# Kernel tuning notes

Measured on AMD Instinct MI355X. Metric: run time of the kernel, lower is better.

## Reference

```python
import jax, jax.numpy as jnp
import numpy as np

B, N, D, H, DEPTH = 2, 2048, 768, 12, 4
DH = D // H
SCALE = DH ** -0.5
EPS = 1e-5
FF = 4 * D


def layer_norm(x, w, b):
    m = jnp.mean(x, axis=-1, keepdims=True)
    v = jnp.mean((x - m) ** 2, axis=-1, keepdims=True)
    return (x - m) * jax.lax.rsqrt(v + EPS) * w + b


def to_heads(t):  # [b, n, D] -> [b, H, n, DH]
    b, n, _ = t.shape
    return t.reshape(b, n, H, DH).transpose(0, 2, 1, 3)


def merge_heads(t):  # [b, H, n, DH] -> [b, n, D]
    b, h, n, dh = t.shape
    return t.transpose(0, 2, 1, 3).reshape(b, n, D)


def attend(q, k, v, bias):
    s = jnp.einsum('bhid,bhjd->bhij', q, k) * SCALE + bias
    a = jax.nn.softmax(s, axis=-1)
    return merge_heads(jnp.einsum('bhij,bhjd->bhid', a, v))


def setup_inputs():
    key = jax.random.key(0)
    ks = iter(jax.random.split(key, 16))

    def p(shape, scale=0.02):
        return jax.random.normal(next(ks), shape, dtype=jnp.float32) * scale

    inp = {
        'x': jax.random.normal(next(ks), (B, N, D), dtype=jnp.float32),
        'context': jax.random.normal(next(ks), (B, N, D), dtype=jnp.float32),
        'relative_position_bias': jax.random.normal(next(ks), (1, H, N, N), dtype=jnp.float32) * 0.02,
        # self-attn params (stacked over depth)
        'ln1_w': jnp.ones((DEPTH, D), jnp.float32), 'ln1_b': jnp.zeros((DEPTH, D), jnp.float32),
        'w_qkv': p((DEPTH, D, 3 * D)),
        'w_so': p((DEPTH, D, D)), 'b_so': jnp.zeros((DEPTH, D), jnp.float32),
        # cross-attn params (shared LN applied to x and context, as in source)
        'ln2_w': jnp.ones((DEPTH, D), jnp.float32), 'ln2_b': jnp.zeros((DEPTH, D), jnp.float32),
        'w_q': p((DEPTH, D, D)), 'w_k': p((DEPTH, D, D)), 'w_v': p((DEPTH, D, D)),
        'w_co': p((DEPTH, D, D)), 'b_co': jnp.zeros((DEPTH, D), jnp.float32),
        # FFN params
        'ln3_w': jnp.ones((DEPTH, D), jnp.float32), 'ln3_b': jnp.zeros((DEPTH, D), jnp.float32),
        'w_f1': p((DEPTH, D, FF)), 'b_f1': jnp.zeros((DEPTH, FF), jnp.float32),
        'w_f2': p((DEPTH, FF, D)), 'b_f2': jnp.zeros((DEPTH, D), jnp.float32),
        # final norm
        'lnout_w': jnp.ones((D,), jnp.float32), 'lnout_b': jnp.zeros((D,), jnp.float32),
    }
    return inp


def reference(x, context, relative_position_bias,
              ln1_w, ln1_b, w_qkv, w_so, b_so,
              ln2_w, ln2_b, w_q, w_k, w_v, w_co, b_co,
              ln3_w, ln3_b, w_f1, b_f1, w_f2, b_f2,
              lnout_w, lnout_b):
    bias = relative_position_bias
    for i in range(DEPTH):
        # self-attention block (pre-norm, residual)
        xn = layer_norm(x, ln1_w[i], ln1_b[i])
        q, k, v = jnp.split(xn @ w_qkv[i], 3, axis=-1)
        o = attend(to_heads(q), to_heads(k), to_heads(v), bias)
        x = o @ w_so[i] + b_so[i] + x
        # cross-attention block (input_norm shared for x and context)
        xn = layer_norm(x, ln2_w[i], ln2_b[i])
        cn = layer_norm(context, ln2_w[i], ln2_b[i])
        o = attend(to_heads(xn @ w_q[i]), to_heads(cn @ w_k[i]), to_heads(cn @ w_v[i]), bias)
        x = o @ w_co[i] + b_co[i] + x
        # FFN block
        xn = layer_norm(x, ln3_w[i], ln3_b[i])
        h = jax.nn.gelu(xn @ w_f1[i] + b_f1[i], approximate=False)
        x = h @ w_f2[i] + b_f2[i] + x
    return layer_norm(x, lnout_w, lnout_b)
```

## Files before the change

### kernel.cpp

```cpp
#include <hip/hip_runtime.h>
#include <cstdint>
#include <cstddef>

#define DEV static __device__ __forceinline__

typedef float  f32x4 __attribute__((ext_vector_type(4)));
typedef short  s16x8 __attribute__((ext_vector_type(8)));
typedef unsigned short u16;
typedef unsigned short u16x2 __attribute__((ext_vector_type(2)));
typedef unsigned short u16x4 __attribute__((ext_vector_type(4)));
typedef __bf16 bf16x8 __attribute__((ext_vector_type(8)));

#define LOG2E 1.4426950408889634f
#define QSCALE_CONST 0.18033688011112042f

DEV float bf2f(u16 v){ union { unsigned u; float f; } x; x.u = ((unsigned)v) << 16; return x.f; }
DEV u16 f2bf(float f){ return __builtin_bit_cast(u16, (__bf16)f); }

DEV float fexp2(float x){
#if __has_builtin(__builtin_amdgcn_exp2f)
  return __builtin_amdgcn_exp2f(x);
#else
  return exp2f(x);
#endif
}

DEV f32x4 mfma16(s16x8 a, s16x8 b, f32x4 c){
  return __builtin_amdgcn_mfma_f32_16x16x32_bf16(
      __builtin_bit_cast(bf16x8, a), __builtin_bit_cast(bf16x8, b), c, 0, 0, 0);
}

DEV void gld16(const void* g, void* l){
  __builtin_amdgcn_global_load_lds(
      (const __attribute__((address_space(1))) void*)(uintptr_t)g,
      (__attribute__((address_space(3))) void*)(unsigned)(uintptr_t)l,
      16, 0, 0);
}

__global__ void __launch_bounds__(256)
transpose_cvt(const float* __restrict__ src, u16* __restrict__ dst, int K, int N,
              size_t dzstride){
  int z = blockIdx.z;
  src += (size_t)z * K * N;
  dst += (size_t)z * dzstride;
  __shared__ float t[32][33];
  int n0 = blockIdx.x * 32, k0 = blockIdx.y * 32;
#pragma unroll
  for (int i = 0; i < 4; ++i)
    t[threadIdx.y + 8*i][threadIdx.x] = src[(size_t)(k0 + threadIdx.y + 8*i) * N + n0 + threadIdx.x];
  __syncthreads();
#pragma unroll
  for (int i = 0; i < 4; ++i)
    dst[(size_t)(n0 + threadIdx.y + 8*i) * K + k0 + threadIdx.x] = f2bf(t[threadIdx.x][threadIdx.y + 8*i]);
}

__global__ void __launch_bounds__(256)
cvt_bias(const float* __restrict__ in, u16* __restrict__ out){
  size_t i = ((size_t)blockIdx.x * 256 + threadIdx.x) * 4;
  f32x4 v = *(const f32x4*)(in + i);
  u16x4 o;
#pragma unroll
  for (int j = 0; j < 4; ++j) o[j] = f2bf(v[j] * LOG2E);
  *(u16x4*)(out + i) = o;
}

template<typename OUT>
__global__ void __launch_bounds__(256)
ln_kernel(const float* __restrict__ x0, const float* __restrict__ x1,
          const float* __restrict__ w, const float* __restrict__ bsh,
          OUT* __restrict__ o0, OUT* __restrict__ o1){
  int row = blockIdx.x, tid = threadIdx.x;
  const float* xr; OUT* orow;
  if (row < 4096){ xr = x0 + (size_t)row * 768; orow = o0 + (size_t)row * 768; }
  else           { xr = x1 + (size_t)(row - 4096) * 768; orow = o1 + (size_t)(row - 4096) * 768; }
  float v0 = xr[tid], v1 = xr[tid + 256], v2 = xr[tid + 512];
  float s = v0 + v1 + v2, s2 = v0*v0 + v1*v1 + v2*v2;
#pragma unroll
  for (int off = 1; off < 64; off <<= 1){ s += __shfl_xor(s, off); s2 += __shfl_xor(s2, off); }
  __shared__ float red[8];
  int wid = tid >> 6;
  if ((tid & 63) == 0){ red[wid] = s; red[wid + 4] = s2; }
  __syncthreads();
  s  = red[0] + red[1] + red[2] + red[3];
  s2 = red[4] + red[5] + red[6] + red[7];
  float m = s * (1.f/768.f);
  float var = s2 * (1.f/768.f) - m * m;
  float rstd = rsqrtf(var + 1e-5f);
#pragma unroll
  for (int i = 0; i < 3; ++i){
    int c = tid + 256 * i;
    float vv = (i == 0 ? v0 : (i == 1 ? v1 : v2));
    float o = (vv - m) * rstd * w[c] + bsh[c];
    if constexpr (sizeof(OUT) == 2) orow[c] = f2bf(o);
    else                            orow[c] = o;
  }
}

template<int BN, int EPI>
__global__ void __launch_bounds__(256)
gemm_bf16(const u16* __restrict__ A, int lda, const u16* __restrict__ Bt, int ldb,
          int nk, u16* __restrict__ Cb, float* __restrict__ Cf, int ldc,
          const float* __restrict__ bias, const float* __restrict__ resid,
          const u16* __restrict__ A2, const u16* __restrict__ Bt2){
  constexpr int NT = BN / 32;
  __shared__ u16 As[2][128 * 32];
  __shared__ u16 Bs[2][BN * 32];
  float colscale = 1.0f;
  if constexpr (EPI == 4){
    const int z = blockIdx.z;
    if (z == 0){ colscale = QSCALE_CONST; }
    else { A = A2; Bt = Bt2 + (size_t)(z - 1) * 768 * 768; }
    Cb += z * 768;
  }
  const int tid = threadIdx.x, w = tid >> 6, lane = tid & 63;
  const int l16 = lane & 15, g = lane >> 4;
  const int m0 = blockIdx.x * 128, n0 = blockIdx.y * BN;
  const int wm = (w >> 1) * 64, wn = (w & 1) * (BN / 2);
  f32x4 acc[4][NT] = {};

  const int L0 = w * 1024 + lane * 16;
  const int L1 = (w + 4) * 1024 + lane * 16;
  const u16* a0 = A + (size_t)(m0 + (L0 >> 6)) * lda + ((L0 & 63) >> 1);
  const u16* a1 = A + (size_t)(m0 + (L1 >> 6)) * lda + ((L1 & 63) >> 1);
  const u16* b0; const u16* b1 = nullptr;
  if constexpr (BN == 128){
    b0 = Bt + (size_t)(n0 + (L0 >> 6)) * ldb + ((L0 & 63) >> 1);
    b1 = Bt + (size_t)(n0 + (L1 >> 6)) * ldb + ((L1 & 63) >> 1);
  } else {
    const int Lb = tid * 16;
    b0 = Bt + (size_t)(n0 + (Lb >> 6)) * ldb + ((Lb & 63) >> 1);
  }

  {
    char* ab = (char*)As[0]; char* bb = (char*)Bs[0];
    gld16(a0, ab + w * 1024); gld16(a1, ab + (w + 4) * 1024);
    if constexpr (BN == 128){ gld16(b0, bb + w * 1024); gld16(b1, bb + (w + 4) * 1024); }
    else                    { gld16(b0, bb + w * 1024); }
  }
  __syncthreads();

  int cb = 0;
  for (int kt = 0; kt < nk; ++kt){
    if (kt + 1 < nk){
      const int k1 = (kt + 1) * 32;
      char* ab = (char*)As[cb ^ 1]; char* bb = (char*)Bs[cb ^ 1];
      gld16(a0 + k1, ab + w * 1024); gld16(a1 + k1, ab + (w + 4) * 1024);
      if constexpr (BN == 128){ gld16(b0 + k1, bb + w * 1024); gld16(b1 + k1, bb + (w + 4) * 1024); }
      else                    { gld16(b0 + k1, bb + w * 1024); }
    }

    const u16* Ab = As[cb]; const u16* Bb = Bs[cb];
    s16x8 af[4], bfv[NT];
#pragma unroll
    for (int mi = 0; mi < 4; ++mi)
      af[mi] = *(const s16x8*)(Ab + (wm + mi*16 + l16) * 32 + 8 * g);
#pragma unroll
    for (int ni = 0; ni < NT; ++ni)
      bfv[ni] = *(const s16x8*)(Bb + (wn + ni*16 + l16) * 32 + 8 * g);
#pragma unroll
    for (int mi = 0; mi < 4; ++mi)
#pragma unroll
      for (int ni = 0; ni < NT; ++ni)
        acc[mi][ni] = mfma16(af[mi], bfv[ni], acc[mi][ni]);

    __syncthreads();
    cb ^= 1;
  }

#pragma unroll
  for (int mi = 0; mi < 4; ++mi){
    const int rg = m0 + wm + mi*16 + 4*g;
#pragma unroll
    for (int ni = 0; ni < NT; ++ni){
      const int col = n0 + wn + ni*16 + l16;
      f32x4 v = acc[mi][ni];
#pragma unroll
      for (int r = 0; r < 4; ++r){
        const int row = rg + r;
        if constexpr (EPI == 0){
          Cb[(size_t)row * ldc + col] = f2bf(v[r]);
        } else if constexpr (EPI == 1){
          Cf[(size_t)row * ldc + col] = v[r] + bias[col] + resid[(size_t)row * ldc + col];
        } else if constexpr (EPI == 2){
          float t = v[r] + bias[col];
          float ge = 0.5f * t * (1.0f + erff(t * 0.7071067811865476f));
          Cb[(size_t)row * ldc + col] = f2bf(ge);
        } else if constexpr (EPI == 3){
          float sc = (col < 768) ? QSCALE_CONST : 1.0f;
          Cb[(size_t)row * ldc + col] = f2bf(v[r] * sc);
        } else {
          Cb[(size_t)row * ldc + col] = f2bf(v[r] * colscale);
        }
      }
    }
  }
}

__global__ void __launch_bounds__(256)
attn_kernel(const u16* __restrict__ qkv, const u16* __restrict__ bias, u16* __restrict__ out){
  __shared__ __align__(16) u16 Ks[2][4096];
  __shared__ __align__(16) u16 Vt[2][4096];
  __shared__ __align__(16) u16 Pl[4][1024];

  const int tid = threadIdx.x, w = tid >> 6, lane = tid & 63;
  const int l16 = lane & 15, g = lane >> 4;
  const int qt = blockIdx.x, h = blockIdx.y, b = blockIdx.z;
  const int rowbase = b * 2048, q0 = qt * 64;

  const int ci0 = w * 64 + lane, ci1 = ci0 + 256;
  const int r0 = ci0 >> 3, sc0 = ci0 & 7, r1 = ci1 >> 3, sc1 = ci1 & 7;
  const u16* kp0 = qkv + (size_t)(rowbase + r0) * 2304 + 768 + h * 64 + (((sc0 ^ (r0 & 7)) & 7) << 3);
  const u16* kp1 = qkv + (size_t)(rowbase + r1) * 2304 + 768 + h * 64 + (((sc1 ^ (r1 & 7)) & 7) << 3);
  const int dh0 = (tid & 31) * 2, vs = tid >> 5;
  const u16* vp = qkv + (size_t)(rowbase + vs * 8) * 2304 + 1536 + h * 64 + dh0;
  u16x2 vr[8];
  const u16* bptr = bias + ((size_t)h * 2048 + q0 + w * 16 + l16) * 2048 + 4 * g;
  u16x4 brc[4], brn[4];

  const u16* qrow = qkv + (size_t)(rowbase + q0 + w * 16 + l16) * 2304 + h * 64;
  s16x8 qf0 = *(const s16x8*)(qrow + 8 * g);
  s16x8 qf1 = *(const s16x8*)(qrow + 32 + 8 * g);

  f32x4 oacc[4] = {};
  float mrun = -3.0e38f, lrun = 0.f;
  const int sw = l16 & 7;

  {
    char* kb = (char*)Ks[0] + w * 1024;
    gld16(kp0, kb); gld16(kp1, kb + 4096);
#pragma unroll
    for (int i = 0; i < 8; ++i) vr[i] = *(const u16x2*)(vp + (size_t)i * 2304);
#pragma unroll
    for (int mi = 0; mi < 4; ++mi) brc[mi] = *(const u16x4*)(bptr + 16 * mi);
    s16x8 vA, vB;
#pragma unroll
    for (int j = 0; j < 8; ++j){ vA[j] = (short)vr[j][0]; vB[j] = (short)vr[j][1]; }
    *(s16x8*)(Vt[0] + dh0 * 64 + ((vs ^ (dh0 & 7)) << 3)) = vA;
    *(s16x8*)(Vt[0] + (dh0 + 1) * 64 + ((vs ^ ((dh0 + 1) & 7)) << 3)) = vB;
  }
  __syncthreads();

  for (int t = 0; t < 32; ++t){
    const int cb = t & 1;
    if (t < 31){
      const size_t koff = (size_t)(t + 1) * 64 * 2304;
      char* kb = (char*)Ks[cb ^ 1] + w * 1024;
      gld16(kp0 + koff, kb); gld16(kp1 + koff, kb + 4096);
      const u16* p = vp + koff;
#pragma unroll
      for (int i = 0; i < 8; ++i) vr[i] = *(const u16x2*)(p + (size_t)i * 2304);
      const u16* bp = bptr + (t + 1) * 64;
#pragma unroll
      for (int mi = 0; mi < 4; ++mi) brn[mi] = *(const u16x4*)(bp + 16 * mi);
    }

    f32x4 st[4];
#pragma unroll
    for (int mi = 0; mi < 4; ++mi){
      const int row = l16 + 16 * mi;
      s16x8 kf0 = *(const s16x8*)(Ks[cb] + row * 64 + ((g ^ sw) << 3));
      s16x8 kf1 = *(const s16x8*)(Ks[cb] + row * 64 + (((g + 4) ^ sw) << 3));
      f32x4 z = {};
      z = mfma16(kf0, qf0, z);
      st[mi] = mfma16(kf1, qf1, z);
    }

    float tmax = -3.0e38f;
#pragma unroll
    for (int mi = 0; mi < 4; ++mi){
#pragma unroll
      for (int r = 0; r < 4; ++r){
        float v = st[mi][r] + bf2f(brc[mi][r]);
        st[mi][r] = v;
        tmax = fmaxf(tmax, v);
      }
    }
    tmax = fmaxf(tmax, __shfl_xor(tmax, 16));
    tmax = fmaxf(tmax, __shfl_xor(tmax, 32));
    if (!__all(tmax <= mrun + 8.f)){
      float mnew = fmaxf(mrun, tmax);
      float al = fexp2(mrun - mnew);
      mrun = mnew;
      lrun *= al;
#pragma unroll
      for (int r = 0; r < 4; ++r){
        float aq = __shfl(al, 4 * g + r);
#pragma unroll
        for (int ni = 0; ni < 4; ++ni) oacc[ni][r] *= aq;
      }
    }
    float ssum = 0.f;
#pragma unroll
    for (int mi = 0; mi < 4; ++mi){
      u16x4 pk;
#pragma unroll
      for (int r = 0; r < 4; ++r){
        float pv = fexp2(st[mi][r] - mrun);
        ssum += pv;
        pk[r] = f2bf(pv);
      }
      *(u16x4*)(Pl[w] + l16 * 64 + (((2*mi + (g >> 1)) ^ sw) << 3) + 4 * (g & 1)) = pk;
    }
    ssum += __shfl_xor(ssum, 16);
    ssum += __shfl_xor(ssum, 32);
    lrun += ssum;

#pragma unroll
    for (int ks2 = 0; ks2 < 2; ++ks2){
      s16x8 pf = *(const s16x8*)(Pl[w] + l16 * 64 + (((4*ks2 + g) ^ sw) << 3));
#pragma unroll
      for (int ni = 0; ni < 4; ++ni){
        const int dh = l16 + 16 * ni;
        s16x8 vf = *(const s16x8*)(Vt[cb] + dh * 64 + (((4*ks2 + g) ^ sw) << 3));
        oacc[ni] = mfma16(pf, vf, oacc[ni]);
      }
    }

    if (t < 31){
      s16x8 vA, vB;
#pragma unroll
      for (int j = 0; j < 8; ++j){ vA[j] = (short)vr[j][0]; vB[j] = (short)vr[j][1]; }
      *(s16x8*)(Vt[cb ^ 1] + dh0 * 64 + ((vs ^ (dh0 & 7)) << 3)) = vA;
      *(s16x8*)(Vt[cb ^ 1] + (dh0 + 1) * 64 + ((vs ^ ((dh0 + 1) & 7)) << 3)) = vB;
#pragma unroll
      for (int mi = 0; mi < 4; ++mi) brc[mi] = brn[mi];
    }
    __syncthreads();
  }

#pragma unroll
  for (int r = 0; r < 4; ++r){
    float lq = __shfl(lrun, 4 * g + r);
    float inv = 1.0f / lq;
    const int row = rowbase + q0 + w * 16 + 4 * g + r;
#pragma unroll
    for (int ni = 0; ni < 4; ++ni)
      out[(size_t)row * 768 + h * 64 + l16 + 16 * ni] = f2bf(oacc[ni][r] * inv);
  }
}

extern "C" void kernel_launch(void* const* d_in, const int* in_sizes, int n_in,
                              void* d_out, int out_size, void* d_ws, size_t ws_size,
                              hipStream_t stream){
  const float* in_x    = (const float*)d_in[0];
  const float* in_ctx  = (const float*)d_in[1];
  const float* in_bias = (const float*)d_in[2];
  const float* ln1_w = (const float*)d_in[3];
  const float* ln1_b = (const float*)d_in[4];
  const float* w_qkv = (const float*)d_in[5];
  const float* w_so  = (const float*)d_in[6];
  const float* b_so  = (const float*)d_in[7];
  const float* ln2_w = (const float*)d_in[8];
  const float* ln2_b = (const float*)d_in[9];
  const float* w_q   = (const float*)d_in[10];
  const float* w_k   = (const float*)d_in[11];
  const float* w_v   = (const float*)d_in[12];
  const float* w_co  = (const float*)d_in[13];
  const float* b_co  = (const float*)d_in[14];
  const float* ln3_w = (const float*)d_in[15];
  const float* ln3_b = (const float*)d_in[16];
  const float* w_f1  = (const float*)d_in[17];
  const float* b_f1  = (const float*)d_in[18];
  const float* w_f2  = (const float*)d_in[19];
  const float* b_f2  = (const float*)d_in[20];
  const float* lnout_w = (const float*)d_in[21];
  const float* lnout_b = (const float*)d_in[22];

  char* p = (char*)d_ws;
  float* xbuf  = (float*)p;  p += 4096ll * 768 * 4;
  u16* xn      = (u16*)p;    p += 4096ll * 768 * 2;
  u16* cn      = (u16*)p;    p += 4096ll * 768 * 2;
  u16* qkvb    = (u16*)p;    p += 4096ll * 2304 * 2;
  u16* attO    = (u16*)p;    p += 4096ll * 768 * 2;
  u16* ffh     = (u16*)p;    p += 4096ll * 3072 * 2;
  u16* wqkvT   = (u16*)p;    p += 4ll * 2304 * 768 * 2;
  u16* wsoT    = (u16*)p;    p += 4ll * 768 * 768 * 2;
  u16* wqT     = (u16*)p;    p += 4ll * 768 * 768 * 2;
  u16* wkvT    = (u16*)p;    p += 4ll * 1536 * 768 * 2;
  u16* wcoT    = (u16*)p;    p += 4ll * 768 * 768 * 2;
  u16* wf1T    = (u16*)p;    p += 4ll * 3072 * 768 * 2;
  u16* wf2T    = (u16*)p;    p += 4ll * 768 * 3072 * 2;
  u16* biasbf  = (u16*)p;    p += 12ll * 2048 * 2048 * 2;

  hipMemcpyAsync(xbuf, in_x, 4096ll * 768 * 4, hipMemcpyDeviceToDevice, stream);

  const dim3 tb(32, 8);
  transpose_cvt<<<dim3(72, 24, 4), tb, 0, stream>>>(w_qkv, wqkvT, 768, 2304, 2304ll*768);
  transpose_cvt<<<dim3(24, 24, 4), tb, 0, stream>>>(w_so,  wsoT,  768, 768,  768ll*768);
  transpose_cvt<<<dim3(24, 24, 4), tb, 0, stream>>>(w_q,   wqT,   768, 768,  768ll*768);
  transpose_cvt<<<dim3(24, 24, 4), tb, 0, stream>>>(w_k,   wkvT,             768, 768, 1536ll*768);
  transpose_cvt<<<dim3(24, 24, 4), tb, 0, stream>>>(w_v,   wkvT + 768ll*768, 768, 768, 1536ll*768);
  transpose_cvt<<<dim3(24, 24, 4), tb, 0, stream>>>(w_co,  wcoT,  768, 768,  768ll*768);
  transpose_cvt<<<dim3(96, 24, 4), tb, 0, stream>>>(w_f1,  wf1T,  768, 3072, 3072ll*768);
  transpose_cvt<<<dim3(24, 96, 4), tb, 0, stream>>>(w_f2,  wf2T,  3072, 768, 768ll*3072);
  cvt_bias<<<49152, 256, 0, stream>>>(in_bias, biasbf);

  const dim3 ag(32, 12, 2);
  for (int i = 0; i < 4; ++i){
    ln_kernel<u16><<<4096, 256, 0, stream>>>(xbuf, nullptr, ln1_w + i*768, ln1_b + i*768, xn, nullptr);
    gemm_bf16<128,3><<<dim3(32, 18), 256, 0, stream>>>(xn, 768, wqkvT + (size_t)i*2304*768, 768, 24,
                                                       qkvb, nullptr, 2304, nullptr, nullptr, nullptr, nullptr);
    attn_kernel<<<ag, 256, 0, stream>>>(qkvb, biasbf, attO);
    gemm_bf16<64,1><<<dim3(32, 12), 256, 0, stream>>>(attO, 768, wsoT + (size_t)i*768*768, 768, 24,
                                                      nullptr, xbuf, 768, b_so + i*768, xbuf, nullptr, nullptr);
    ln_kernel<u16><<<8192, 256, 0, stream>>>(xbuf, in_ctx, ln2_w + i*768, ln2_b + i*768, xn, cn);
    gemm_bf16<64,4><<<dim3(32, 12, 3), 256, 0, stream>>>(xn, 768, wqT + (size_t)i*768*768, 768, 24,
                                                         qkvb, nullptr, 2304, nullptr, nullptr,
                                                         cn, wkvT + (size_t)i*1536*768);
    attn_kernel<<<ag, 256, 0, stream>>>(qkvb, biasbf, attO);
    gemm_bf16<64,1><<<dim3(32, 12), 256, 0, stream>>>(attO, 768, wcoT + (size_t)i*768*768, 768, 24,
                                                      nullptr, xbuf, 768, b_co + i*768, xbuf, nullptr, nullptr);
    ln_kernel<u16><<<4096, 256, 0, stream>>>(xbuf, nullptr, ln3_w + i*768, ln3_b + i*768, xn, nullptr);
    gemm_bf16<128,2><<<dim3(32, 24), 256, 0, stream>>>(xn, 768, wf1T + (size_t)i*3072*768, 768, 24,
                                                       ffh, nullptr, 3072, b_f1 + i*3072, nullptr, nullptr, nullptr);
    gemm_bf16<64,1><<<dim3(32, 12), 256, 0, stream>>>(ffh, 3072, wf2T + (size_t)i*768*3072, 3072, 96,
                                                      nullptr, xbuf, 768, b_f2 + i*768, xbuf, nullptr, nullptr);
  }
  ln_kernel<float><<<4096, 256, 0, stream>>>(xbuf, nullptr, lnout_w, lnout_b, (float*)d_out, nullptr);
}
```

Before: 1.459 ms.

## Split-K output GEMMs with fused reduce+residual+LayerNorm, pre-tiled bias, hoisted context LN

The output-projection and FFN2 GEMMs now run as 2-way split-K writing fp32 partials. A new red_ln kernel sums the partials, adds the bias and residual, and applies the next LayerNorm in one pass with one wave per row. The relative position bias is pre-tiled into a per-tile layout so the attention kernel loads it with contiguous 16-byte reads. The context LayerNorm for all four layers is computed once before the loop, and the QKV/FFN1 GEMMs use 64x128 tiles for more blocks. These changes cut kernel launches and global round trips but add extra fp32 partial traffic and workspace.

```diff
diff --git a/kernel.cpp b/kernel.cpp
--- a/kernel.cpp
+++ b/kernel.cpp
@@ -9,6 +9,7 @@
 typedef unsigned short u16;
 typedef unsigned short u16x2 __attribute__((ext_vector_type(2)));
 typedef unsigned short u16x4 __attribute__((ext_vector_type(4)));
+typedef unsigned short u16x8 __attribute__((ext_vector_type(8)));
 typedef __bf16 bf16x8 __attribute__((ext_vector_type(8)));
 
 #define LOG2E 1.4426950408889634f
@@ -55,55 +56,113 @@
 }
 
 __global__ void __launch_bounds__(256)
-cvt_bias(const float* __restrict__ in, u16* __restrict__ out){
-  size_t i = ((size_t)blockIdx.x * 256 + threadIdx.x) * 4;
-  f32x4 v = *(const f32x4*)(in + i);
-  u16x4 o;
-#pragma unroll
-  for (int j = 0; j < 4; ++j) o[j] = f2bf(v[j] * LOG2E);
-  *(u16x4*)(out + i) = o;
+cvt_biasT(const float* __restrict__ in, u16* __restrict__ out){
+  const int kvt = blockIdx.x, qt = blockIdx.y, h = blockIdx.z, tid = threadIdx.x;
+  const int q  = qt * 64 + ((tid >> 6) << 4) + (tid & 15);
+  const int c0 = kvt * 64 + ((tid >> 4) & 3) * 4;
+  const float* src = in + ((size_t)h * 2048 + q) * 2048;
+  u16x8 o0, o1;
+#pragma unroll
+  for (int mi = 0; mi < 4; ++mi){
+    f32x4 v = *(const f32x4*)(src + c0 + mi * 16);
+#pragma unroll
+    for (int r = 0; r < 4; ++r){
+      u16 bv = f2bf(v[r] * LOG2E);
+      if (mi < 2) o0[(mi & 1) * 4 + r] = bv; else o1[(mi & 1) * 4 + r] = bv;
+    }
+  }
+  u16* dst = out + ((size_t)(h * 32 + qt) * 32 + kvt) * 4096 + tid * 16;
+  *(u16x8*)dst = o0;
+  *(u16x8*)(dst + 8) = o1;
+}
+
+__global__ void __launch_bounds__(256)
+lnv(const float* __restrict__ x, const float* __restrict__ w, const float* __restrict__ b,
+    u16* __restrict__ out){
+  const int wv = threadIdx.x >> 6, lane = threadIdx.x & 63;
+  const float* wz = w + blockIdx.y * 768;
+  const float* bz = b + blockIdx.y * 768;
+  out += (size_t)blockIdx.y * 4096 * 768;
+  const int row = blockIdx.x * 4 + wv;
+  const float* xr = x + (size_t)row * 768;
+  f32x4 t[3]; float s = 0.f, s2 = 0.f;
+#pragma unroll
+  for (int c = 0; c < 3; ++c){
+    t[c] = *(const f32x4*)(xr + c * 256 + lane * 4);
+#pragma unroll
+    for (int j = 0; j < 4; ++j){ s += t[c][j]; s2 += t[c][j] * t[c][j]; }
+  }
+#pragma unroll
+  for (int off = 1; off < 64; off <<= 1){ s += __shfl_xor(s, off); s2 += __shfl_xor(s2, off); }
+  float m = s * (1.f/768.f);
+  float rstd = rsqrtf(s2 * (1.f/768.f) - m * m + 1e-5f);
+#pragma unroll
+  for (int c = 0; c < 3; ++c){
+    const int col = c * 256 + lane * 4;
+    f32x4 wv4 = *(const f32x4*)(wz + col);
+    f32x4 bv4 = *(const f32x4*)(bz + col);
+    u16x4 o;
+#pragma unroll
+    for (int j = 0; j < 4; ++j) o[j] = f2bf((t[c][j] - m) * rstd * wv4[j] + bv4[j]);
+    *(u16x4*)(out + (size_t)row * 768 + col) = o;
+  }
 }
 
 template<typename OUT>
 __global__ void __launch_bounds__(256)
-ln_kernel(const float* __restrict__ x0, const float* __restrict__ x1,
-          const float* __restrict__ w, const float* __restrict__ bsh,
-          OUT* __restrict__ o0, OUT* __restrict__ o1){
-  int row = blockIdx.x, tid = threadIdx.x;
-  const float* xr; OUT* orow;
-  if (row < 4096){ xr = x0 + (size_t)row * 768; orow = o0 + (size_t)row * 768; }
-  else           { xr = x1 + (size_t)(row - 4096) * 768; orow = o1 + (size_t)(row - 4096) * 768; }
-  float v0 = xr[tid], v1 = xr[tid + 256], v2 = xr[tid + 512];
-  float s = v0 + v1 + v2, s2 = v0*v0 + v1*v1 + v2*v2;
+red_ln(const float* __restrict__ p, const float* __restrict__ biasrow,
+       float* __restrict__ xbuf, OUT* __restrict__ out,
+       const float* __restrict__ lw, const float* __restrict__ lb){
+  const int wv = threadIdx.x >> 6, lane = threadIdx.x & 63;
+  const int row = blockIdx.x * 4 + wv;
+  const float* p0 = p + (size_t)row * 768;
+  const float* p1 = p0 + 4096ll * 768;
+  float* xr = xbuf + (size_t)row * 768;
+  f32x4 t[3]; float s = 0.f, s2 = 0.f;
+#pragma unroll
+  for (int c = 0; c < 3; ++c){
+    const int col = c * 256 + lane * 4;
+    f32x4 v0 = *(const f32x4*)(p0 + col);
+    f32x4 v1 = *(const f32x4*)(p1 + col);
+    f32x4 bv = *(const f32x4*)(biasrow + col);
+    f32x4 xv = *(const f32x4*)(xr + col);
+    f32x4 v = v0 + v1 + bv + xv;
+    *(f32x4*)(xr + col) = v;
+    t[c] = v;
+#pragma unroll
+    for (int j = 0; j < 4; ++j){ s += v[j]; s2 += v[j] * v[j]; }
+  }
 #pragma unroll
   for (int off = 1; off < 64; off <<= 1){ s += __shfl_xor(s, off); s2 += __shfl_xor(s2, off); }
-  __shared__ float red[8];
-  int wid = tid >> 6;
-  if ((tid & 63) == 0){ red[wid] = s; red[wid + 4] = s2; }
-  __syncthreads();
-  s  = red[0] + red[1] + red[2] + red[3];
-  s2 = red[4] + red[5] + red[6] + red[7];
   float m = s * (1.f/768.f);
-  float var = s2 * (1.f/768.f) - m * m;
-  float rstd = rsqrtf(var + 1e-5f);
-#pragma unroll
-  for (int i = 0; i < 3; ++i){
-    int c = tid + 256 * i;
-    float vv = (i == 0 ? v0 : (i == 1 ? v1 : v2));
-    float o = (vv - m) * rstd * w[c] + bsh[c];
-    if constexpr (sizeof(OUT) == 2) orow[c] = f2bf(o);
-    else                            orow[c] = o;
-  }
-}
-
-template<int BN, int EPI>
+  float rstd = rsqrtf(s2 * (1.f/768.f) - m * m + 1e-5f);
+#pragma unroll
+  for (int c = 0; c < 3; ++c){
+    const int col = c * 256 + lane * 4;
+    f32x4 wv4 = *(const f32x4*)(lw + col);
+    f32x4 bv4 = *(const f32x4*)(lb + col);
+    if constexpr (sizeof(OUT) == 2){
+      u16x4 o;
+#pragma unroll
+      for (int j = 0; j < 4; ++j) o[j] = f2bf((t[c][j] - m) * rstd * wv4[j] + bv4[j]);
+      *(u16x4*)((u16*)out + (size_t)row * 768 + col) = o;
+    } else {
+      f32x4 o;
+#pragma unroll
+      for (int j = 0; j < 4; ++j) o[j] = (t[c][j] - m) * rstd * wv4[j] + bv4[j];
+      *(f32x4*)((float*)out + (size_t)row * 768 + col) = o;
+    }
+  }
+}
+
+template<int BM, int BN, int EPI>
 __global__ void __launch_bounds__(256)
 gemm_bf16(const u16* __restrict__ A, int lda, const u16* __restrict__ Bt, int ldb,
           int nk, u16* __restrict__ Cb, float* __restrict__ Cf, int ldc,
-          const float* __restrict__ bias, const float* __restrict__ resid,
+          const float* __restrict__ bias,
           const u16* __restrict__ A2, const u16* __restrict__ Bt2){
-  constexpr int NT = BN / 32;
-  __shared__ u16 As[2][128 * 32];
+  constexpr int MT = BM / 32, NT = BN / 32;
+  __shared__ u16 As[2][BM * 32];
   __shared__ u16 Bs[2][BN * 32];
   float colscale = 1.0f;
   if constexpr (EPI == 4){
@@ -112,30 +171,29 @@
     else { A = A2; Bt = Bt2 + (size_t)(z - 1) * 768 * 768; }
     Cb += z * 768;
   }
+  if constexpr (EPI == 5){
+    const int z = blockIdx.z;
+    A  += (size_t)z * nk * 32;
+    Bt += (size_t)z * nk * 32;
+    Cf += (size_t)z * 4096 * 768;
+  }
   const int tid = threadIdx.x, w = tid >> 6, lane = tid & 63;
   const int l16 = lane & 15, g = lane >> 4;
-  const int m0 = blockIdx.x * 128, n0 = blockIdx.y * BN;
-  const int wm = (w >> 1) * 64, wn = (w & 1) * (BN / 2);
-  f32x4 acc[4][NT] = {};
-
-  const int L0 = w * 1024 + lane * 16;
-  const int L1 = (w + 4) * 1024 + lane * 16;
-  const u16* a0 = A + (size_t)(m0 + (L0 >> 6)) * lda + ((L0 & 63) >> 1);
-  const u16* a1 = A + (size_t)(m0 + (L1 >> 6)) * lda + ((L1 & 63) >> 1);
-  const u16* b0; const u16* b1 = nullptr;
-  if constexpr (BN == 128){
-    b0 = Bt + (size_t)(n0 + (L0 >> 6)) * ldb + ((L0 & 63) >> 1);
-    b1 = Bt + (size_t)(n0 + (L1 >> 6)) * ldb + ((L1 & 63) >> 1);
-  } else {
-    const int Lb = tid * 16;
-    b0 = Bt + (size_t)(n0 + (Lb >> 6)) * ldb + ((Lb & 63) >> 1);
-  }
+  const int m0 = blockIdx.x * BM, n0 = blockIdx.y * BN;
+  const int wm = (w >> 1) * (BM / 2), wn = (w & 1) * (BN / 2);
+  f32x4 acc[MT][NT] = {};
+
+  const u16* a0 = A + (size_t)(m0 + (tid >> 2)) * lda + (tid & 3) * 8;
+  const u16* a1 = (BM == 128) ? A + (size_t)(m0 + (tid >> 2) + 64) * lda + (tid & 3) * 8 : nullptr;
+  const u16* b0 = Bt + (size_t)(n0 + (tid >> 2)) * ldb + (tid & 3) * 8;
+  const u16* b1 = (BN == 128) ? Bt + (size_t)(n0 + (tid >> 2) + 64) * ldb + (tid & 3) * 8 : nullptr;
 
   {
     char* ab = (char*)As[0]; char* bb = (char*)Bs[0];
-    gld16(a0, ab + w * 1024); gld16(a1, ab + (w + 4) * 1024);
-    if constexpr (BN == 128){ gld16(b0, bb + w * 1024); gld16(b1, bb + (w + 4) * 1024); }
-    else                    { gld16(b0, bb + w * 1024); }
+    gld16(a0, ab + w * 1024);
+    if constexpr (BM == 128) gld16(a1, ab + 4096 + w * 1024);
+    gld16(b0, bb + w * 1024);
+    if constexpr (BN == 128) gld16(b1, bb + 4096 + w * 1024);
   }
   __syncthreads();
 
@@ -144,31 +202,30 @@
     if (kt + 1 < nk){
       const int k1 = (kt + 1) * 32;
       char* ab = (char*)As[cb ^ 1]; char* bb = (char*)Bs[cb ^ 1];
-      gld16(a0 + k1, ab + w * 1024); gld16(a1 + k1, ab + (w + 4) * 1024);
-      if constexpr (BN == 128){ gld16(b0 + k1, bb + w * 1024); gld16(b1 + k1, bb + (w + 4) * 1024); }
-      else                    { gld16(b0 + k1, bb + w * 1024); }
-    }
-
+      gld16(a0 + k1, ab + w * 1024);
+      if constexpr (BM == 128) gld16(a1 + k1, ab + 4096 + w * 1024);
+      gld16(b0 + k1, bb + w * 1024);
+      if constexpr (BN == 128) gld16(b1 + k1, bb + 4096 + w * 1024);
+    }
     const u16* Ab = As[cb]; const u16* Bb = Bs[cb];
-    s16x8 af[4], bfv[NT];
-#pragma unroll
-    for (int mi = 0; mi < 4; ++mi)
+    s16x8 af[MT], bfv[NT];
+#pragma unroll
+    for (int mi = 0; mi < MT; ++mi)
       af[mi] = *(const s16x8*)(Ab + (wm + mi*16 + l16) * 32 + 8 * g);
 #pragma unroll
     for (int ni = 0; ni < NT; ++ni)
       bfv[ni] = *(const s16x8*)(Bb + (wn + ni*16 + l16) * 32 + 8 * g);
 #pragma unroll
-    for (int mi = 0; mi < 4; ++mi)
+    for (int mi = 0; mi < MT; ++mi)
 #pragma unroll
       for (int ni = 0; ni < NT; ++ni)
         acc[mi][ni] = mfma16(af[mi], bfv[ni], acc[mi][ni]);
-
     __syncthreads();
     cb ^= 1;
   }
 
 #pragma unroll
-  for (int mi = 0; mi < 4; ++mi){
+  for (int mi = 0; mi < MT; ++mi){
     const int rg = m0 + wm + mi*16 + 4*g;
 #pragma unroll
     for (int ni = 0; ni < NT; ++ni){
@@ -177,19 +234,17 @@
 #pragma unroll
       for (int r = 0; r < 4; ++r){
         const int row = rg + r;
-        if constexpr (EPI == 0){
-          Cb[(size_t)row * ldc + col] = f2bf(v[r]);
-        } else if constexpr (EPI == 1){
-          Cf[(size_t)row * ldc + col] = v[r] + bias[col] + resid[(size_t)row * ldc + col];
-        } else if constexpr (EPI == 2){
+        if constexpr (EPI == 2){
           float t = v[r] + bias[col];
           float ge = 0.5f * t * (1.0f + erff(t * 0.7071067811865476f));
           Cb[(size_t)row * ldc + col] = f2bf(ge);
         } else if constexpr (EPI == 3){
           float sc = (col < 768) ? QSCALE_CONST : 1.0f;
           Cb[(size_t)row * ldc + col] = f2bf(v[r] * sc);
+        } else if constexpr (EPI == 4){
+          Cb[(size_t)row * ldc + col] = f2bf(v[r] * colscale);
         } else {
-          Cb[(size_t)row * ldc + col] = f2bf(v[r] * colscale);
+          Cf[(size_t)row * 768 + col] = v[r];
         }
       }
     }
@@ -197,7 +252,7 @@
 }
 
 __global__ void __launch_bounds__(256)
-attn_kernel(const u16* __restrict__ qkv, const u16* __restrict__ bias, u16* __restrict__ out){
+attn_kernel(const u16* __restrict__ qkv, const u16* __restrict__ biasT, u16* __restrict__ out){
   __shared__ __align__(16) u16 Ks[2][4096];
   __shared__ __align__(16) u16 Vt[2][4096];
   __shared__ __align__(16) u16 Pl[4][1024];
@@ -214,8 +269,8 @@
   const int dh0 = (tid & 31) * 2, vs = tid >> 5;
   const u16* vp = qkv + (size_t)(rowbase + vs * 8) * 2304 + 1536 + h * 64 + dh0;
   u16x2 vr[8];
-  const u16* bptr = bias + ((size_t)h * 2048 + q0 + w * 16 + l16) * 2048 + 4 * g;
-  u16x4 brc[4], brn[4];
+  const u16* bT = biasT + ((size_t)(h * 32 + qt) * 32) * 4096 + tid * 16;
+  u16x8 brA, brB, bnA, bnB;
 
   const u16* qrow = qkv + (size_t)(rowbase + q0 + w * 16 + l16) * 2304 + h * 64;
   s16x8 qf0 = *(const s16x8*)(qrow + 8 * g);
@@ -230,8 +285,8 @@
     gld16(kp0, kb); gld16(kp1, kb + 4096);
 #pragma unroll
     for (int i = 0; i < 8; ++i) vr[i] = *(const u16x2*)(vp + (size_t)i * 2304);
-#pragma unroll
-    for (int mi = 0; mi < 4; ++mi) brc[mi] = *(const u16x4*)(bptr + 16 * mi);
+    brA = *(const u16x8*)(bT);
+    brB = *(const u16x8*)(bT + 8);
     s16x8 vA, vB;
 #pragma unroll
     for (int j = 0; j < 8; ++j){ vA[j] = (short)vr[j][0]; vB[j] = (short)vr[j][1]; }
@@ -249,9 +304,9 @@
       const u16* p = vp + koff;
 #pragma unroll
       for (int i = 0; i < 8; ++i) vr[i] = *(const u16x2*)(p + (size_t)i * 2304);
-      const u16* bp = bptr + (t + 1) * 64;
-#pragma unroll
-      for (int mi = 0; mi < 4; ++mi) brn[mi] = *(const u16x4*)(bp + 16 * mi);
+      const u16* bp = bT + (size_t)(t + 1) * 4096;
+      bnA = *(const u16x8*)(bp);
+      bnB = *(const u16x8*)(bp + 8);
     }
 
     f32x4 st[4];
@@ -270,7 +325,8 @@
     for (int mi = 0; mi < 4; ++mi){
 #pragma unroll
       for (int r = 0; r < 4; ++r){
-        float v = st[mi][r] + bf2f(brc[mi][r]);
+        float bval = bf2f(mi < 2 ? brA[(mi & 1) * 4 + r] : brB[(mi & 1) * 4 + r]);
+        float v = st[mi][r] + bval;
         st[mi][r] = v;
         tmax = fmaxf(tmax, v);
       }
@@ -322,8 +378,7 @@
       for (int j = 0; j < 8; ++j){ vA[j] = (short)vr[j][0]; vB[j] = (short)vr[j][1]; }
       *(s16x8*)(Vt[cb ^ 1] + dh0 * 64 + ((vs ^ (dh0 & 7)) << 3)) = vA;
       *(s16x8*)(Vt[cb ^ 1] + (dh0 + 1) * 64 + ((vs ^ ((dh0 + 1) & 7)) << 3)) = vB;
-#pragma unroll
-      for (int mi = 0; mi < 4; ++mi) brc[mi] = brn[mi];
+      brA = bnA; brB = bnB;
     }
     __syncthreads();
   }
@@ -368,8 +423,9 @@
 
   char* p = (char*)d_ws;
   float* xbuf  = (float*)p;  p += 4096ll * 768 * 4;
+  float* pbuf  = (float*)p;  p += 2ll * 4096 * 768 * 4;
   u16* xn      = (u16*)p;    p += 4096ll * 768 * 2;
-  u16* cn      = (u16*)p;    p += 4096ll * 768 * 2;
+  u16* cn      = (u16*)p;    p += 4ll * 4096 * 768 * 2;
   u16* qkvb    = (u16*)p;    p += 4096ll * 2304 * 2;
   u16* attO    = (u16*)p;    p += 4096ll * 768 * 2;
   u16* ffh     = (u16*)p;    p += 4096ll * 3072 * 2;
@@ -380,7 +436,7 @@
   u16* wcoT    = (u16*)p;    p += 4ll * 768 * 768 * 2;
   u16* wf1T    = (u16*)p;    p += 4ll * 3072 * 768 * 2;
   u16* wf2T    = (u16*)p;    p += 4ll * 768 * 3072 * 2;
-  u16* biasbf  = (u16*)p;    p += 12ll * 2048 * 2048 * 2;
+  u16* biasT   = (u16*)p;    p += 12ll * 2048 * 2048 * 2;
 
   hipMemcpyAsync(xbuf, in_x, 4096ll * 768 * 4, hipMemcpyDeviceToDevice, stream);
 
@@ -393,28 +449,32 @@
   transpose_cvt<<<dim3(24, 24, 4), tb, 0, stream>>>(w_co,  wcoT,  768, 768,  768ll*768);
   transpose_cvt<<<dim3(96, 24, 4), tb, 0, stream>>>(w_f1,  wf1T,  768, 3072, 3072ll*768);
   transpose_cvt<<<dim3(24, 96, 4), tb, 0, stream>>>(w_f2,  wf2T,  3072, 768, 768ll*3072);
-  cvt_bias<<<49152, 256, 0, stream>>>(in_bias, biasbf);
+  cvt_biasT<<<dim3(32, 32, 12), 256, 0, stream>>>(in_bias, biasT);
+  lnv<<<dim3(1024, 4), 256, 0, stream>>>(in_ctx, ln2_w, ln2_b, cn);
+  lnv<<<dim3(1024, 1), 256, 0, stream>>>(xbuf, ln1_w, ln1_b, xn);
 
   const dim3 ag(32, 12, 2);
   for (int i = 0; i < 4; ++i){
-    ln_kernel<u16><<<4096, 256, 0, stream>>>(xbuf, nullptr, ln1_w + i*768, ln1_b + i*768, xn, nullptr);
-    gemm_bf16<128,3><<<dim3(32, 18), 256, 0, stream>>>(xn, 768, wqkvT + (size_t)i*2304*768, 768, 24,
-                                                       qkvb, nullptr, 2304, nullptr, nullptr, nullptr, nullptr);
-    attn_kernel<<<ag, 256, 0, stream>>>(qkvb, biasbf, attO);
-    gemm_bf16<64,1><<<dim3(32, 12), 256, 0, stream>>>(attO, 768, wsoT + (size_t)i*768*768, 768, 24,
-                                                      nullptr, xbuf, 768, b_so + i*768, xbuf, nullptr, nullptr);
-    ln_kernel<u16><<<8192, 256, 0, stream>>>(xbuf, in_ctx, ln2_w + i*768, ln2_b + i*768, xn, cn);
-    gemm_bf16<64,4><<<dim3(32, 12, 3), 256, 0, stream>>>(xn, 768, wqT + (size_t)i*768*768, 768, 24,
-                                                         qkvb, nullptr, 2304, nullptr, nullptr,
-                                                         cn, wkvT + (size_t)i*1536*768);
-    attn_kernel<<<ag, 256, 0, stream>>>(qkvb, biasbf, attO);
-    gemm_bf16<64,1><<<dim3(32, 12), 256, 0, stream>>>(attO, 768, wcoT + (size_t)i*768*768, 768, 24,
-                                                      nullptr, xbuf, 768, b_co + i*768, xbuf, nullptr, nullptr);
-    ln_kernel<u16><<<4096, 256, 0, stream>>>(xbuf, nullptr, ln3_w + i*768, ln3_b + i*768, xn, nullptr);
-    gemm_bf16<128,2><<<dim3(32, 24), 256, 0, stream>>>(xn, 768, wf1T + (size_t)i*3072*768, 768, 24,
-                                                       ffh, nullptr, 3072, b_f1 + i*3072, nullptr, nullptr, nullptr);
-    gemm_bf16<64,1><<<dim3(32, 12), 256, 0, stream>>>(ffh, 3072, wf2T + (size_t)i*768*3072, 3072, 96,
-                                                      nullptr, xbuf, 768, b_f2 + i*768, xbuf, nullptr, nullptr);
-  }
-  ln_kernel<float><<<4096, 256, 0, stream>>>(xbuf, nullptr, lnout_w, lnout_b, (float*)d_out, nullptr);
-}
+    gemm_bf16<64,128,3><<<dim3(64, 18), 256, 0, stream>>>(xn, 768, wqkvT + (size_t)i*2304*768, 768, 24,
+                                                          qkvb, nullptr, 2304, nullptr, nullptr, nullptr);
+    attn_kernel<<<ag, 256, 0, stream>>>(qkvb, biasT, attO);
+    gemm_bf16<128,64,5><<<dim3(32, 12, 2), 256, 0, stream>>>(attO, 768, wsoT + (size_t)i*768*768, 768, 12,
+                                                             nullptr, pbuf, 768, nullptr, nullptr, nullptr);
+    red_ln<u16><<<1024, 256, 0, stream>>>(pbuf, b_so + i*768, xbuf, xn, ln2_w + i*768, ln2_b + i*768);
+    gemm_bf16<64,128,4><<<dim3(64, 6, 3), 256, 0, stream>>>(xn, 768, wqT + (size_t)i*768*768, 768, 24,
+                                                            qkvb, nullptr, 2304, nullptr,
+                                                            cn + (size_t)i*4096*768, wkvT + (size_t)i*1536*768);
+    attn_kernel<<<ag, 256, 0, stream>>>(qkvb, biasT, attO);
+    gemm_bf16<128,64,5><<<dim3(32, 12, 2), 256, 0, stream>>>(attO, 768, wcoT + (size_t)i*768*768, 768, 12,
+                                                             nullptr, pbuf, 768, nullptr, nullptr, nullptr);
+    red_ln<u16><<<1024, 256, 0, stream>>>(pbuf, b_co + i*768, xbuf, xn, ln3_w + i*768, ln3_b + i*768);
+    gemm_bf16<64,128,2><<<dim3(64, 24), 256, 0, stream>>>(xn, 768, wf1T + (size_t)i*3072*768, 768, 24,
+                                                          ffh, nullptr, 3072, b_f1 + i*3072, nullptr, nullptr);
+    gemm_bf16<128,64,5><<<dim3(32, 12, 2), 256, 0, stream>>>(ffh, 3072, wf2T + (size_t)i*768*3072, 3072, 48,
+                                                             nullptr, pbuf, 768, nullptr, nullptr, nullptr);
+    if (i < 3)
+      red_ln<u16><<<1024, 256, 0, stream>>>(pbuf, b_f2 + i*768, xbuf, xn, ln1_w + (i+1)*768, ln1_b + (i+1)*768);
+    else
+      red_ln<float><<<1024, 256, 0, stream>>>(pbuf, b_f2 + i*768, xbuf, (float*)d_out, lnout_w, lnout_b);
+  }
+}
```

Result: faster. 1.419 ms (-2.8%).
